# Kernel optimization log

Measured on AMD Instinct MI355X. Metric: run time of the kernel, lower is better.

Reference implementation:

```python
import jax, jax.numpy as jnp
import numpy as np


def binarize(t):
    # sign binarizer to exactly +/-1 (sign(0) -> +1), matching is_binary_tensor check
    return jnp.where(t >= 0, 1.0, -1.0).astype(t.dtype)


def setup_inputs() -> dict:
    key = jax.random.key(0)
    kx, kw, kb = jax.random.split(key, 3)
    x = jax.random.normal(kx, (32, 256, 56, 56), dtype=jnp.float32)
    weight = jax.random.normal(kw, (256, 256, 3, 3), dtype=jnp.float32)
    bias = jax.random.normal(kb, (256,), dtype=jnp.float32)
    return {"x": x, "weight": weight, "bias": bias}


def reference(x, weight, bias):
    bx = binarize(x)            # [B, Cin, H, W] in {-1, +1}
    bw = binarize(weight)       # [Cout, Cin, kh, kw] in {-1, +1}
    # F.conv2d(stride=1, padding=1, dilation=1, groups=1)
    out = jax.lax.conv_general_dilated(
        bx, bw,
        window_strides=(1, 1),
        padding=((1, 1), (1, 1)),
        dimension_numbers=("NCHW", "OIHW", "NCHW"),
    )
    return out + bias[None, :, None, None]
```

## Files before the change

### kernel.cpp

```cpp
#include <hip/hip_runtime.h>
#include <cstdint>

constexpr int B = 32, C = 256, H = 56, W = 56;
constexpr int HW = H * W;
constexpr int WORDS = 8;
constexpr int TAPS = 9;
constexpr int WPC = TAPS * WORDS;
constexpr int PH = H + 2, PW = W + 2, PHW = PH * PW;

__global__ __launch_bounds__(256) void pad_zero_kernel(uint32_t* __restrict__ px) {
    int idx = blockIdx.x * 256 + threadIdx.x;
    int wd = idx & 7;
    int r = idx >> 3;
    int ring = r % 228;
    int b = r / 228;
    int ph, pwp;
    if (ring < 58)       { ph = 0;              pwp = ring; }
    else if (ring < 116) { ph = 57;             pwp = ring - 58; }
    else if (ring < 172) { ph = 1 + (ring - 116); pwp = 0; }
    else                 { ph = 1 + (ring - 172); pwp = 57; }
    px[((size_t)(b * PH + ph) * PW + pwp) * WORDS + wd] = 0u;
}

__global__ __launch_bounds__(256) void pack_x_kernel(const float* __restrict__ x,
                                                     uint32_t* __restrict__ px) {
    int idx = blockIdx.x * 256 + threadIdx.x;
    int hw4 = idx % 784;
    int r = idx / 784;
    int wd = r & 7;
    int b = r >> 3;
    const float4* xp = reinterpret_cast<const float4*>(x + ((size_t)b * C + wd * 32) * HW) + hw4;
    uint32_t w0 = 0, w1 = 0, w2 = 0, w3 = 0;
    #pragma unroll
    for (int i = 0; i < 32; ++i) {
        float4 v = xp[(size_t)i * (HW / 4)];
        w0 |= (__float_as_uint(v.x) >> 31) << i;
        w1 |= (__float_as_uint(v.y) >> 31) << i;
        w2 |= (__float_as_uint(v.z) >> 31) << i;
        w3 |= (__float_as_uint(v.w) >> 31) << i;
    }
    int hw = hw4 * 4;
    #pragma unroll
    for (int q = 0; q < 4; ++q) {
        int h = (hw + q) / W, w = (hw + q) - h * W;
        uint32_t val = (q == 0) ? w0 : (q == 1) ? w1 : (q == 2) ? w2 : w3;
        px[((size_t)(b * PH + h + 1) * PW + (w + 1)) * WORDS + wd] = val;
    }
}

__global__ __launch_bounds__(256) void pack_w_kernel(const float* __restrict__ wt,
                                                     uint32_t* __restrict__ pw) {
    int gid = blockIdx.x * 256 + threadIdx.x;
    int lane = gid & 63;
    int wv = gid >> 6;
    int pr = wv & 3;
    int ct = wv >> 2;
    int tap = ct % 9;
    int co = ct / 9;
    int ci = pr * 64 + lane;
    float v = wt[((size_t)co * C + ci) * TAPS + tap];
    unsigned long long m = __ballot(v < 0.0f);
    if (lane == 0) {
        pw[(size_t)co * WPC + tap * WORDS + pr * 2]     = (uint32_t)m;
        pw[(size_t)co * WPC + tap * WORDS + pr * 2 + 1] = (uint32_t)(m >> 32);
    }
}

__global__ __launch_bounds__(256) void bconv_kernel(const uint32_t* __restrict__ px,
                                                    const uint32_t* __restrict__ pw,
                                                    const float* __restrict__ bias,
                                                    float* __restrict__ out) {
    const int lane = threadIdx.x & 63;
    const int wid = threadIdx.x >> 6;
    const int co = wid * 64 + lane;
    const int hwbase = blockIdx.x * 64;
    const int b = blockIdx.y;

    uint32_t wreg[WPC];
    {
        const uint4* wp = reinterpret_cast<const uint4*>(pw + (size_t)co * WPC);
        #pragma unroll
        for (int i = 0; i < 18; ++i) {
            uint4 v = wp[i];
            wreg[i * 4 + 0] = v.x; wreg[i * 4 + 1] = v.y;
            wreg[i * 4 + 2] = v.z; wreg[i * 4 + 3] = v.w;
        }
    }
    uint32_t tp[TAPS];
    #pragma unroll
    for (int t = 0; t < TAPS; ++t) {
        uint32_t s = 0;
        #pragma unroll
        for (int k = 0; k < WORDS; ++k) s += __popc(wreg[t * WORDS + k]);
        tp[t] = s;
    }

    const float basep = 2304.0f + bias[co];
    float* outrow = out + ((size_t)b * C + co) * HW + hwbase;

    #pragma unroll 1
    for (int p4 = 0; p4 < 16; ++p4) {
        float o0, o1, o2, o3;
        #pragma unroll
        for (int q = 0; q < 4; ++q) {
            const int p = p4 * 4 + q;
            const int hw = hwbase + p;
            const int h = hw / W;
            const int w = hw - h * W;
            const uint32_t* rp = px + ((size_t)(b * PH + h) * PW + w) * WORDS;
            uint32_t a0 = 0, a1 = 0, a2 = 0, a3 = 0;
            #pragma unroll
            for (int row = 0; row < 3; ++row) {
                const uint32_t* rr = rp + row * (PW * WORDS);
                #pragma unroll
                for (int c = 0; c < 3; ++c) {
                    const int t = row * 3 + c;
                    a0 += __popc(rr[c * 8 + 0] ^ wreg[t * 8 + 0]);
                    a1 += __popc(rr[c * 8 + 1] ^ wreg[t * 8 + 1]);
                    a2 += __popc(rr[c * 8 + 2] ^ wreg[t * 8 + 2]);
                    a3 += __popc(rr[c * 8 + 3] ^ wreg[t * 8 + 3]);
                    a0 += __popc(rr[c * 8 + 4] ^ wreg[t * 8 + 4]);
                    a1 += __popc(rr[c * 8 + 5] ^ wreg[t * 8 + 5]);
                    a2 += __popc(rr[c * 8 + 6] ^ wreg[t * 8 + 6]);
                    a3 += __popc(rr[c * 8 + 7] ^ wreg[t * 8 + 7]);
                }
            }
            const uint32_t total = (a0 + a1) + (a2 + a3);
            float base2 = basep;
            if (h == 0 || h == H - 1 || w == 0 || w == W - 1) {
                uint32_t s = 0;
                int ninv = 0;
                #pragma unroll
                for (int t = 0; t < TAPS; ++t) {
                    const int dh = t / 3, dw = t % 3;
                    const bool inv = (h == 0 && dh == 0) || (h == H - 1 && dh == 2) ||
                                     (w == 0 && dw == 0) || (w == W - 1 && dw == 2);
                    if (inv) { s += tp[t]; ++ninv; }
                }
                base2 = basep + (float)(2 * (int)s - 256 * ninv);
            }
            const float res = fmaf(-2.0f, (float)(int)total, base2);
            if (q == 0) o0 = res; else if (q == 1) o1 = res;
            else if (q == 2) o2 = res; else o3 = res;
        }
        reinterpret_cast<float4*>(outrow)[p4] = make_float4(o0, o1, o2, o3);
    }
}

extern "C" void kernel_launch(void* const* d_in, const int* in_sizes, int n_in,
                              void* d_out, int out_size, void* d_ws, size_t ws_size,
                              hipStream_t stream) {
    const float* x = (const float*)d_in[0];
    const float* wt = (const float*)d_in[1];
    const float* bias = (const float*)d_in[2];
    float* out = (float*)d_out;

    uint32_t* px = (uint32_t*)d_ws;
    uint32_t* pw = px + (size_t)B * PHW * WORDS;

    pad_zero_kernel<<<(B * 228 * WORDS) / 256, 256, 0, stream>>>(px);
    pack_x_kernel<<<(B * WORDS * (HW / 4)) / 256, 256, 0, stream>>>(x, px);
    pack_w_kernel<<<(C * TAPS * 4 * 64) / 256, 256, 0, stream>>>(wt, pw);

    dim3 grid(HW / 64, B);
    bconv_kernel<<<grid, 256, 0, stream>>>(px, pw, bias, out);
}
```

Measured before the change: 421.5 us.

## Stage conv outputs through shared memory for coalesced 64-byte row stores

The conv kernel now computes 16 output pixels per thread per chunk and writes them into a padded shared-memory tile. It then rereads the tile transposed, so four consecutive threads store a contiguous 64-byte segment of one output channel row. Before, each lane wrote a float4 to a different channel row, which scattered the stores. The change adds shared-memory traffic, two barriers per chunk and more registers for the 16-value array, and it requests 4 blocks per CU via launch bounds.

```diff
diff --git a/kernel.cpp b/kernel.cpp
--- a/kernel.cpp
+++ b/kernel.cpp
@@ -7,6 +7,7 @@
 constexpr int TAPS = 9;
 constexpr int WPC = TAPS * WORDS;
 constexpr int PH = H + 2, PW = W + 2, PHW = PH * PW;
+constexpr int RSTRIDE = 20;
 
 __global__ __launch_bounds__(256) void pad_zero_kernel(uint32_t* __restrict__ px) {
     int idx = blockIdx.x * 256 + threadIdx.x;
@@ -66,15 +67,17 @@
     }
 }
 
-__global__ __launch_bounds__(256) void bconv_kernel(const uint32_t* __restrict__ px,
-                                                    const uint32_t* __restrict__ pw,
-                                                    const float* __restrict__ bias,
-                                                    float* __restrict__ out) {
+__global__ __launch_bounds__(256, 4) void bconv_kernel(const uint32_t* __restrict__ px,
+                                                       const uint32_t* __restrict__ pw,
+                                                       const float* __restrict__ bias,
+                                                       float* __restrict__ out) {
     const int lane = threadIdx.x & 63;
     const int wid = threadIdx.x >> 6;
     const int co = wid * 64 + lane;
     const int hwbase = blockIdx.x * 64;
     const int b = blockIdx.y;
+
+    __shared__ float res[256 * RSTRIDE];
 
     uint32_t wreg[WPC];
     {
@@ -94,17 +97,15 @@
         for (int k = 0; k < WORDS; ++k) s += __popc(wreg[t * WORDS + k]);
         tp[t] = s;
     }
-
     const float basep = 2304.0f + bias[co];
-    float* outrow = out + ((size_t)b * C + co) * HW + hwbase;
 
     #pragma unroll 1
-    for (int p4 = 0; p4 < 16; ++p4) {
-        float o0, o1, o2, o3;
+    for (int chunk = 0; chunk < 4; ++chunk) {
+        const int pbase = hwbase + chunk * 16;
+        float o[16];
         #pragma unroll
-        for (int q = 0; q < 4; ++q) {
-            const int p = p4 * 4 + q;
-            const int hw = hwbase + p;
+        for (int q = 0; q < 16; ++q) {
+            const int hw = pbase + q;
             const int h = hw / W;
             const int w = hw - h * W;
             const uint32_t* rp = px + ((size_t)(b * PH + h) * PW + w) * WORDS;
@@ -139,11 +140,25 @@
                 }
                 base2 = basep + (float)(2 * (int)s - 256 * ninv);
             }
-            const float res = fmaf(-2.0f, (float)(int)total, base2);
-            if (q == 0) o0 = res; else if (q == 1) o1 = res;
-            else if (q == 2) o2 = res; else o3 = res;
+            o[q] = fmaf(-2.0f, (float)(int)total, base2);
         }
-        reinterpret_cast<float4*>(outrow)[p4] = make_float4(o0, o1, o2, o3);
+
+        __syncthreads();
+        #pragma unroll
+        for (int qq = 0; qq < 16; qq += 4) {
+            *reinterpret_cast<float4*>(&res[co * RSTRIDE + qq]) =
+                make_float4(o[qq], o[qq + 1], o[qq + 2], o[qq + 3]);
+        }
+        __syncthreads();
+
+        #pragma unroll
+        for (int i = 0; i < 4; ++i) {
+            const int t = threadIdx.x;
+            const int co2 = (i * 256 + t) >> 2;
+            const int pp = (t & 3) << 2;
+            float4 v = *reinterpret_cast<const float4*>(&res[co2 * RSTRIDE + pp]);
+            *reinterpret_cast<float4*>(out + ((size_t)b * C + co2) * HW + pbase + pp) = v;
+        }
     }
 }
 
```

Result: slower. 461.1 us (+9.4%).

## Restructure binary conv to hold input window in registers and loop over channels

Applied to the files above, without the earlier changes.

Each thread now computes two adjacent output pixels. It keeps a 3x4 packed input window in registers and loops over 64 output channels, reading the weights as wave-uniform loads, where before each thread held one channel's weights and reloaded input pixels. Border correction terms move into a precomputed per-channel table built by a new small kernel, and the pack_x thread mapping is reordered for more coalesced writes. The aim is to reuse input bits across neighbouring pixels and cut redundant global loads, at the cost of more registers, a different grid shape and an extra launch.

```diff
diff --git a/kernel.cpp b/kernel.cpp
--- a/kernel.cpp
+++ b/kernel.cpp
@@ -25,10 +25,10 @@
 __global__ __launch_bounds__(256) void pack_x_kernel(const float* __restrict__ x,
                                                      uint32_t* __restrict__ px) {
     int idx = blockIdx.x * 256 + threadIdx.x;
-    int hw4 = idx % 784;
-    int r = idx / 784;
-    int wd = r & 7;
-    int b = r >> 3;
+    int wd = idx & 7;
+    int r = idx >> 3;
+    int hw4 = r % 784;
+    int b = r / 784;
     const float4* xp = reinterpret_cast<const float4*>(x + ((size_t)b * C + wd * 32) * HW) + hw4;
     uint32_t w0 = 0, w1 = 0, w2 = 0, w3 = 0;
     #pragma unroll
@@ -40,12 +40,12 @@
         w3 |= (__float_as_uint(v.w) >> 31) << i;
     }
     int hw = hw4 * 4;
-    #pragma unroll
-    for (int q = 0; q < 4; ++q) {
-        int h = (hw + q) / W, w = (hw + q) - h * W;
-        uint32_t val = (q == 0) ? w0 : (q == 1) ? w1 : (q == 2) ? w2 : w3;
-        px[((size_t)(b * PH + h + 1) * PW + (w + 1)) * WORDS + wd] = val;
-    }
+    int h = hw / W, w = hw - h * W;
+    uint32_t* dst = px + ((size_t)(b * PH + h + 1) * PW + (w + 1)) * WORDS + wd;
+    dst[0]  = w0;
+    dst[8]  = w1;
+    dst[16] = w2;
+    dst[24] = w3;
 }
 
 __global__ __launch_bounds__(256) void pack_w_kernel(const float* __restrict__ wt,
@@ -66,84 +66,110 @@
     }
 }
 
-__global__ __launch_bounds__(256) void bconv_kernel(const uint32_t* __restrict__ px,
-                                                    const uint32_t* __restrict__ pw,
-                                                    const float* __restrict__ bias,
-                                                    float* __restrict__ out) {
-    const int lane = threadIdx.x & 63;
-    const int wid = threadIdx.x >> 6;
-    const int co = wid * 64 + lane;
-    const int hwbase = blockIdx.x * 64;
-    const int b = blockIdx.y;
-
-    uint32_t wreg[WPC];
-    {
-        const uint4* wp = reinterpret_cast<const uint4*>(pw + (size_t)co * WPC);
-        #pragma unroll
-        for (int i = 0; i < 18; ++i) {
-            uint4 v = wp[i];
-            wreg[i * 4 + 0] = v.x; wreg[i * 4 + 1] = v.y;
-            wreg[i * 4 + 2] = v.z; wreg[i * 4 + 3] = v.w;
-        }
-    }
+__global__ __launch_bounds__(256) void ctab_kernel(const uint32_t* __restrict__ pw,
+                                                   const float* __restrict__ bias,
+                                                   uint32_t* __restrict__ ctab,
+                                                   float* __restrict__ btab) {
+    int co = threadIdx.x;
     uint32_t tp[TAPS];
     #pragma unroll
     for (int t = 0; t < TAPS; ++t) {
         uint32_t s = 0;
         #pragma unroll
-        for (int k = 0; k < WORDS; ++k) s += __popc(wreg[t * WORDS + k]);
+        for (int k = 0; k < WORDS; ++k) s += __popc(pw[(size_t)co * WPC + t * 8 + k]);
         tp[t] = s;
     }
+    uint32_t* c8 = ctab + (size_t)co * 8;
+    c8[0] = tp[0] + tp[1] + tp[2];
+    c8[1] = tp[6] + tp[7] + tp[8];
+    c8[2] = tp[0] + tp[3] + tp[6];
+    c8[3] = tp[2] + tp[5] + tp[8];
+    c8[4] = tp[0]; c8[5] = tp[2]; c8[6] = tp[6]; c8[7] = tp[8];
+    btab[co] = 2304.0f + bias[co];
+}
 
-    const float basep = 2304.0f + bias[co];
-    float* outrow = out + ((size_t)b * C + co) * HW + hwbase;
+__global__ __launch_bounds__(64, 3) void bconv_kernel(const uint32_t* __restrict__ px,
+                                                      const uint32_t* __restrict__ pw,
+                                                      const uint32_t* __restrict__ ctab,
+                                                      const float* __restrict__ btab,
+                                                      float* __restrict__ out) {
+    const int lane = threadIdx.x;
+    const int cobase = blockIdx.y * 64;
+    const int b = blockIdx.z;
+    int hw = blockIdx.x * 128 + lane * 2;
+    const bool active = (hw < HW);
+    if (!active) hw = HW - 2;
+    const int h = hw / W;
+    const int w = hw - h * W;
+
+    uint32_t win[3][4][8];
+    #pragma unroll
+    for (int r = 0; r < 3; ++r) {
+        const uint4* rp = reinterpret_cast<const uint4*>(
+            px + ((size_t)(b * PH + h + r) * PW + w) * WORDS);
+        #pragma unroll
+        for (int c = 0; c < 4; ++c) {
+            uint4 lo = rp[c * 2], hi = rp[c * 2 + 1];
+            win[r][c][0] = lo.x; win[r][c][1] = lo.y; win[r][c][2] = lo.z; win[r][c][3] = lo.w;
+            win[r][c][4] = hi.x; win[r][c][5] = hi.y; win[r][c][6] = hi.z; win[r][c][7] = hi.w;
+        }
+    }
+
+    const bool bh0 = (h == 0), bh1 = (h == H - 1);
+    const bool bw0 = (w == 0), bw1 = (w + 1 == W - 1);
+    const uint32_t mT = bh0 ? ~0u : 0u;
+    const uint32_t mB = bh1 ? ~0u : 0u;
+    const uint32_t mLa = bw0 ? ~0u : 0u;
+    const uint32_t mRb = bw1 ? ~0u : 0u;
+    const uint32_t mCa = (mT | mB) & mLa;
+    const uint32_t mCb = (mT | mB) & mRb;
+    const int nva = 3 * ((int)bh0 + (int)bh1 + (int)bw0) - (mCa ? 1 : 0);
+    const int nvb = 3 * ((int)bh0 + (int)bh1 + (int)bw1) - (mCb ? 1 : 0);
+    const float fa = -256.0f * (float)nva;
+    const float fb = -256.0f * (float)nvb;
+
+    float* op = out + ((size_t)b * C + cobase) * HW + hw;
 
     #pragma unroll 1
-    for (int p4 = 0; p4 < 16; ++p4) {
-        float o0, o1, o2, o3;
+    for (int j = 0; j < 64; ++j) {
+        const uint32_t* wr = pw + (size_t)(cobase + j) * WPC;
+        uint32_t a0 = 0, a1 = 0, a2 = 0, a3 = 0;
+        uint32_t b0 = 0, b1 = 0, b2 = 0, b3 = 0;
         #pragma unroll
-        for (int q = 0; q < 4; ++q) {
-            const int p = p4 * 4 + q;
-            const int hw = hwbase + p;
-            const int h = hw / W;
-            const int w = hw - h * W;
-            const uint32_t* rp = px + ((size_t)(b * PH + h) * PW + w) * WORDS;
-            uint32_t a0 = 0, a1 = 0, a2 = 0, a3 = 0;
+        for (int r = 0; r < 3; ++r) {
             #pragma unroll
-            for (int row = 0; row < 3; ++row) {
-                const uint32_t* rr = rp + row * (PW * WORDS);
-                #pragma unroll
-                for (int c = 0; c < 3; ++c) {
-                    const int t = row * 3 + c;
-                    a0 += __popc(rr[c * 8 + 0] ^ wreg[t * 8 + 0]);
-                    a1 += __popc(rr[c * 8 + 1] ^ wreg[t * 8 + 1]);
-                    a2 += __popc(rr[c * 8 + 2] ^ wreg[t * 8 + 2]);
-                    a3 += __popc(rr[c * 8 + 3] ^ wreg[t * 8 + 3]);
-                    a0 += __popc(rr[c * 8 + 4] ^ wreg[t * 8 + 4]);
-                    a1 += __popc(rr[c * 8 + 5] ^ wreg[t * 8 + 5]);
-                    a2 += __popc(rr[c * 8 + 6] ^ wreg[t * 8 + 6]);
-                    a3 += __popc(rr[c * 8 + 7] ^ wreg[t * 8 + 7]);
-                }
+            for (int c = 0; c < 3; ++c) {
+                const int t = r * 3 + c;
+                a0 += __popc(win[r][c][0]     ^ wr[t * 8 + 0]);
+                a1 += __popc(win[r][c][1]     ^ wr[t * 8 + 1]);
+                a2 += __popc(win[r][c][2]     ^ wr[t * 8 + 2]);
+                a3 += __popc(win[r][c][3]     ^ wr[t * 8 + 3]);
+                a0 += __popc(win[r][c][4]     ^ wr[t * 8 + 4]);
+                a1 += __popc(win[r][c][5]     ^ wr[t * 8 + 5]);
+                a2 += __popc(win[r][c][6]     ^ wr[t * 8 + 6]);
+                a3 += __popc(win[r][c][7]     ^ wr[t * 8 + 7]);
+                b0 += __popc(win[r][c + 1][0] ^ wr[t * 8 + 0]);
+                b1 += __popc(win[r][c + 1][1] ^ wr[t * 8 + 1]);
+                b2 += __popc(win[r][c + 1][2] ^ wr[t * 8 + 2]);
+                b3 += __popc(win[r][c + 1][3] ^ wr[t * 8 + 3]);
+                b0 += __popc(win[r][c + 1][4] ^ wr[t * 8 + 4]);
+                b1 += __popc(win[r][c + 1][5] ^ wr[t * 8 + 5]);
+                b2 += __popc(win[r][c + 1][6] ^ wr[t * 8 + 6]);
+                b3 += __popc(win[r][c + 1][7] ^ wr[t * 8 + 7]);
             }
-            const uint32_t total = (a0 + a1) + (a2 + a3);
-            float base2 = basep;
-            if (h == 0 || h == H - 1 || w == 0 || w == W - 1) {
-                uint32_t s = 0;
-                int ninv = 0;
-                #pragma unroll
-                for (int t = 0; t < TAPS; ++t) {
-                    const int dh = t / 3, dw = t % 3;
-                    const bool inv = (h == 0 && dh == 0) || (h == H - 1 && dh == 2) ||
-                                     (w == 0 && dw == 0) || (w == W - 1 && dw == 2);
-                    if (inv) { s += tp[t]; ++ninv; }
-                }
-                base2 = basep + (float)(2 * (int)s - 256 * ninv);
-            }
-            const float res = fmaf(-2.0f, (float)(int)total, base2);
-            if (q == 0) o0 = res; else if (q == 1) o1 = res;
-            else if (q == 2) o2 = res; else o3 = res;
         }
-        reinterpret_cast<float4*>(outrow)[p4] = make_float4(o0, o1, o2, o3);
+        const uint32_t ta = (a0 + a1) + (a2 + a3);
+        const uint32_t tb = (b0 + b1) + (b2 + b3);
+
+        const uint32_t* c8 = ctab + (size_t)(cobase + j) * 8;
+        const uint32_t sv = (c8[0] & mT) + (c8[1] & mB);
+        const uint32_t Sa = sv + (c8[2] & mLa) - ((bh0 ? c8[4] : c8[6]) & mCa);
+        const uint32_t Sb = sv + (c8[3] & mRb) - ((bh0 ? c8[5] : c8[7]) & mCb);
+        const float bb = btab[cobase + j];
+        const float oa = fmaf(-2.0f, (float)((int)ta - (int)Sa), bb + fa);
+        const float ob = fmaf(-2.0f, (float)((int)tb - (int)Sb), bb + fb);
+        if (active)
+            *reinterpret_cast<float2*>(op + (size_t)j * HW) = make_float2(oa, ob);
     }
 }
 
@@ -157,11 +183,14 @@
 
     uint32_t* px = (uint32_t*)d_ws;
     uint32_t* pw = px + (size_t)B * PHW * WORDS;
+    uint32_t* ctab = pw + (size_t)C * WPC;
+    float* btab = (float*)(ctab + (size_t)C * 8);
 
     pad_zero_kernel<<<(B * 228 * WORDS) / 256, 256, 0, stream>>>(px);
     pack_x_kernel<<<(B * WORDS * (HW / 4)) / 256, 256, 0, stream>>>(x, px);
     pack_w_kernel<<<(C * TAPS * 4 * 64) / 256, 256, 0, stream>>>(wt, pw);
+    ctab_kernel<<<1, 256, 0, stream>>>(pw, bias, ctab, btab);
 
-    dim3 grid(HW / 64, B);
-    bconv_kernel<<<grid, 256, 0, stream>>>(px, pw, bias, out);
+    dim3 grid((HW / 2 + 63) / 64, C / 64, B);
+    bconv_kernel<<<grid, 64, 0, stream>>>(px, pw, ctab, btab, out);
 }
```

Result: faster. 360.4 us (-14.5%).
